# Kernel tuning notes

Hardware: AMD Instinct MI355X
Metric: run time of the kernel (lower is better)

The kernel has to match this reference:

```python
import jax, jax.numpy as jnp
import numpy as np

MARGIN = 1.0
SAFE_RADIUS = 4.0
B, C, H, W = 16, 48, 64, 64
N_CORR = 2048


def _normalize(x, eps=1e-12):
    # F.normalize(x, dim=0): L2-normalize over the channel axis
    return x / jnp.maximum(jnp.linalg.norm(x, axis=0, keepdims=True), eps)


def _grid_positions(h, w):
    i, j = jnp.meshgrid(jnp.arange(h, dtype=jnp.float32),
                        jnp.arange(w, dtype=jnp.float32), indexing='ij')
    return jnp.stack([i.reshape(-1), j.reshape(-1)], axis=0)


def _per_image(df1, df2, att1, att2, ids, fp2):
    c, h1, w1 = df1.shape
    _, h2, w2 = df2.shape
    all_d1 = _normalize(df1.reshape(c, -1))   # [c, h1*w1]
    all_d2 = _normalize(df2.reshape(c, -1))   # [c, h2*w2]

    d1 = all_d1[:, ids]                       # [c, n] gathered anchors
    s1 = att1.reshape(-1)[ids]                # [n]
    d2 = _normalize(df2[:, fp2[0], fp2[1]])   # [c, n] gathered positives

    positive_distance = 2.0 - 2.0 * jnp.sum(d1 * d2, axis=0)  # [n]

    # hard-negative mining in image 2
    grid2 = _grid_positions(h2, w2)           # [2, h2*w2]
    pd2 = jnp.max(jnp.abs(fp2.astype(jnp.float32)[:, :, None] - grid2[:, None, :]), axis=0)
    out2 = (pd2 > SAFE_RADIUS).astype(df1.dtype)            # [n, h2*w2]
    dm2 = 2.0 - 2.0 * jnp.einsum('cn,cm->nm', d1, all_d2)   # [n, h2*w2]
    neg2 = jnp.min(dm2 + (1.0 - out2) * 10.0, axis=1)       # [n]

    # hard-negative mining in image 1
    grid1 = _grid_positions(h1, w1)
    fp1 = grid1[:, ids]                                      # [2, n]
    pd1 = jnp.max(jnp.abs(fp1[:, :, None] - grid1[:, None, :]), axis=0)
    out1 = (pd1 > SAFE_RADIUS).astype(df1.dtype)
    dm1 = 2.0 - 2.0 * jnp.einsum('cn,cm->nm', d2, all_d1)
    neg1 = jnp.min(dm1 + (1.0 - out1) * 10.0, axis=1)

    diff = positive_distance - jnp.minimum(neg1, neg2)
    s2 = att2[0, fp2[0], fp2[1]]
    w = s1 * s2
    return jnp.sum(w * jax.nn.relu(MARGIN + diff)) / jnp.sum(w)


def setup_inputs() -> dict:
    key = jax.random.key(0)
    k1, k2, k3, k4, k5, k6 = jax.random.split(key, 6)
    return {
        'x1_encoded': jax.random.normal(k1, (B, C, H, W), dtype=jnp.float32),
        'x2_encoded': jax.random.normal(k2, (B, C, H, W), dtype=jnp.float32),
        'attentions1': jax.random.uniform(k3, (B, 1, H, W), dtype=jnp.float32),
        'attentions2': jax.random.uniform(k4, (B, 1, H, W), dtype=jnp.float32),
        'ids': jax.random.randint(k5, (B, N_CORR), 0, H * W),
        'fmap_pos2': jax.random.randint(k6, (B, 2, N_CORR), 0, H),
    }


def reference(x1_encoded, x2_encoded, attentions1, attentions2, ids, fmap_pos2):
    per_image = jax.vmap(_per_image)(x1_encoded, x2_encoded, attentions1,
                                     attentions2, ids, fmap_pos2)
    return jnp.mean(per_image).reshape(1)
```

## Files before the change

### kernel.cpp

```cpp
#include <hip/hip_runtime.h>
#include <stdint.h>

#define BB 16
#define HW 4096
#define NC 2048
#define KHW 72
#define KB 144

typedef __attribute__((ext_vector_type(8))) __bf16 bf16x8;
typedef __attribute__((ext_vector_type(8))) short short8;
typedef __attribute__((ext_vector_type(4))) float floatx4;

static __device__ __forceinline__ unsigned short f2bf(float f) {
    unsigned u = __builtin_bit_cast(unsigned, f);
    unsigned r = u + 0x7fffu + ((u >> 16) & 1u);
    return (unsigned short)(r >> 16);
}

#define GLD16(g, l) __builtin_amdgcn_global_load_lds((const __attribute__((address_space(1))) void*)(g), (__attribute__((address_space(3))) void*)(l), 16, 0, 0)
#define GLD4(g, l)  __builtin_amdgcn_global_load_lds((const __attribute__((address_space(1))) void*)(g), (__attribute__((address_space(3))) void*)(l), 4, 0, 0)

__global__ void prep_db(const float* __restrict__ x1, const float* __restrict__ x2,
                        unsigned short* __restrict__ dbp) {
    int gid = blockIdx.x * 256 + threadIdx.x;
    int img = gid >> 16;
    int rem = gid & 65535;
    int b = rem >> 12;
    int p = rem & (HW - 1);
    const float* x = img ? x2 : x1;
    const float* col = x + (size_t)b * 48 * HW + p;
    float v[48]; float s = 0.f;
#pragma unroll
    for (int c = 0; c < 48; ++c) { v[c] = col[c * HW]; s = fmaf(v[c], v[c], s); }
    float r = 1.f / fmaxf(sqrtf(s), 1e-12f);
    unsigned short* dst = dbp + ((size_t)(img * BB + b) * HW + p) * KHW;
#pragma unroll
    for (int ch = 0; ch < 6; ++ch) {
        union { unsigned u[4]; floatx4 f; } pk;
#pragma unroll
        for (int d = 0; d < 4; ++d) {
            int c = ch * 8 + d * 2;
            pk.u[d] = (unsigned)f2bf(v[c] * r) | ((unsigned)f2bf(v[c + 1] * r) << 16);
        }
        *(floatx4*)(dst + ch * 8) = pk.f;
    }
    floatx4 z = {0.f, 0.f, 0.f, 0.f};
#pragma unroll
    for (int ch = 6; ch < 9; ++ch) *(floatx4*)(dst + ch * 8) = z;
}

__global__ void sortq_kernel(const int* __restrict__ ids, const int* __restrict__ fp2,
                             int* __restrict__ perm, int* __restrict__ qcol_s,
                             int* __restrict__ aqpack) {
    int seg = blockIdx.x;
    int dir = seg >> 4, b = seg & 15;
    int tid = threadIdx.x;
    __shared__ int hist[64], base[64];
    if (tid < 64) hist[tid] = 0;
    __syncthreads();
#pragma unroll
    for (int k = 0; k < 8; ++k) {
        int n = k * 256 + tid;
        int idv = ids[b * NC + n];
        int i2 = fp2[b * 2 * NC + n];
        int qi = (dir == 0) ? i2 : (idv >> 6);
        atomicAdd(&hist[qi], 1);
    }
    __syncthreads();
    if (tid == 0) {
        int run = 0;
        for (int k = 0; k < 64; ++k) { base[k] = run; run += hist[k]; }
    }
    __syncthreads();
#pragma unroll
    for (int k = 0; k < 8; ++k) {
        int n = k * 256 + tid;
        int idv = ids[b * NC + n];
        int i2 = fp2[b * 2 * NC + n];
        int j2 = fp2[b * 2 * NC + NC + n];
        int qi, qj, qcol;
        if (dir == 0) { qi = i2; qj = j2; qcol = idv; }
        else          { qi = idv >> 6; qj = idv & 63; qcol = i2 * 64 + j2; }
        int slot = atomicAdd(&base[qi], 1);
        perm[seg * NC + slot] = n;
        qcol_s[seg * NC + slot] = qcol;
        aqpack[seg * NC + slot] = (qi << 8) | qj;
    }
}

static __device__ __forceinline__ void dma_tile(const unsigned char* g, unsigned char* l,
                                                int wave, int lane) {
#pragma unroll
    for (int rr = 0; rr < 4; ++rr)
        GLD16(g + rr * 4096 + wave * 1024 + lane * 16, l + rr * 4096 + wave * 1024);
#pragma unroll
    for (int rr = 0; rr < 2; ++rr)
        GLD4(g + 16384 + rr * 1024 + wave * 256 + lane * 4, l + 16384 + rr * 1024 + wave * 256);
}

__global__ __launch_bounds__(256, 4) void maxscore_mfma(
    const unsigned short* __restrict__ dbp,
    const int* __restrict__ perm, const int* __restrict__ qcol_s,
    const int* __restrict__ aqpack, unsigned int* __restrict__ maxs2enc) {
    __shared__ __align__(16) unsigned char smem[36864];

    int tid = threadIdx.x, wave = tid >> 6, lane = tid & 63;
    int quad = lane >> 4, cl = lane & 15;
    int gid = blockIdx.x;
    int seg = gid & 31, dir = seg >> 4, b = seg & 15;
    int rest = gid >> 5, mtile = rest & 7, nq = rest >> 3;
    int qbase = mtile * 256;
    int dbimg = 1 - dir;

    const unsigned char* dbQ = (const unsigned char*)(dbp + (size_t)(dir * BB + b) * HW * KHW);
    short8 afr[4][2];
#pragma unroll
    for (int t = 0; t < 4; ++t) {
        int slot = qbase + wave * 64 + t * 16 + cl;
        int qc = qcol_s[seg * NC + slot];
        const unsigned char* src = dbQ + (size_t)qc * KB;
        afr[t][0] = *(const short8*)(src + quad * 16);
        afr[t][1] = *(const short8*)(src + 64 + quad * 16);
    }
    float qif[4][4], qjc[4][4];
    float cl_f = (float)cl;
#pragma unroll
    for (int t = 0; t < 4; ++t)
#pragma unroll
        for (int r = 0; r < 4; ++r) {
            int slot = qbase + wave * 64 + t * 16 + quad * 4 + r;
            int ap = aqpack[seg * NC + slot];
            qif[t][r] = (float)(ap >> 8);
            qjc[t][r] = (float)(ap & 255) - cl_f;
        }
    int wb = seg * NC + qbase + wave * 64;
    int qimin = __builtin_amdgcn_readfirstlane(aqpack[wb] >> 8);
    int qimax = __builtin_amdgcn_readfirstlane(aqpack[wb + 63] >> 8);

    const unsigned char* dsrc =
        (const unsigned char*)(dbp + ((size_t)(dbimg * BB + b) * HW + nq * 1024) * KHW);
    dma_tile(dsrc, smem, wave, lane);

    const floatx4 zf = {0.f, 0.f, 0.f, 0.f};
    float mx[4][4];
#pragma unroll
    for (int t = 0; t < 4; ++t)
#pragma unroll
        for (int r = 0; r < 4; ++r) mx[t][r] = -1e30f;

    for (int tile = 0; tile < 8; ++tile) {
        unsigned char* buf = smem + (tile & 1) * 18432;
        __syncthreads();
        if (tile + 1 < 8)
            dma_tile(dsrc + (tile + 1) * 18432, smem + ((tile + 1) & 1) * 18432, wave, lane);
        int mi0 = (nq * 1024 + tile * 128) >> 6;
#pragma unroll
        for (int half = 0; half < 2; ++half) {
            int mi = mi0 + half;
            bool active = (mi >= qimin - 4) && (mi <= qimax + 4);
            if (active) {
                float mi_f = (float)mi;
                bool rowok[4][4];
#pragma unroll
                for (int t = 0; t < 4; ++t)
#pragma unroll
                    for (int r = 0; r < 4; ++r)
                        rowok[t][r] = fabsf(qif[t][r] - mi_f) > 4.0f;
#pragma unroll
                for (int js = 0; js < 4; ++js) {
                    int sub = half * 4 + js;
                    float jj = (float)(js * 16);
                    short8 b0 = *(const short8*)(buf + (sub * 16 + cl) * KB + quad * 16);
                    short8 b1 = *(const short8*)(buf + (sub * 16 + cl) * KB + 64 + quad * 16);
#pragma unroll
                    for (int t = 0; t < 4; ++t) {
                        floatx4 acc = __builtin_amdgcn_mfma_f32_16x16x32_bf16(
                            __builtin_bit_cast(bf16x8, afr[t][0]),
                            __builtin_bit_cast(bf16x8, b0), zf, 0, 0, 0);
                        acc = __builtin_amdgcn_mfma_f32_16x16x32_bf16(
                            __builtin_bit_cast(bf16x8, afr[t][1]),
                            __builtin_bit_cast(bf16x8, b1), acc, 0, 0, 0);
#pragma unroll
                        for (int r = 0; r < 4; ++r) {
                            float dj = qjc[t][r] - jj;
                            bool ok = rowok[t][r] || (fabsf(dj) > 4.0f);
                            mx[t][r] = ok ? fmaxf(mx[t][r], acc[r]) : mx[t][r];
                        }
                    }
                }
            } else {
#pragma unroll
                for (int js = 0; js < 4; ++js) {
                    int sub = half * 4 + js;
                    short8 b0 = *(const short8*)(buf + (sub * 16 + cl) * KB + quad * 16);
                    short8 b1 = *(const short8*)(buf + (sub * 16 + cl) * KB + 64 + quad * 16);
#pragma unroll
                    for (int t = 0; t < 4; ++t) {
                        floatx4 acc = __builtin_amdgcn_mfma_f32_16x16x32_bf16(
                            __builtin_bit_cast(bf16x8, afr[t][0]),
                            __builtin_bit_cast(bf16x8, b0), zf, 0, 0, 0);
                        acc = __builtin_amdgcn_mfma_f32_16x16x32_bf16(
                            __builtin_bit_cast(bf16x8, afr[t][1]),
                            __builtin_bit_cast(bf16x8, b1), acc, 0, 0, 0);
#pragma unroll
                        for (int r = 0; r < 4; ++r)
                            mx[t][r] = fmaxf(mx[t][r], acc[r]);
                    }
                }
            }
        }
    }

#pragma unroll
    for (int t = 0; t < 4; ++t)
#pragma unroll
        for (int r = 0; r < 4; ++r) {
            float v = mx[t][r];
            v = fmaxf(v, __shfl_xor(v, 1, 16));
            v = fmaxf(v, __shfl_xor(v, 2, 16));
            v = fmaxf(v, __shfl_xor(v, 4, 16));
            v = fmaxf(v, __shfl_xor(v, 8, 16));
            mx[t][r] = v;
        }
    if (cl == 0) {
#pragma unroll
        for (int t = 0; t < 4; ++t)
#pragma unroll
            for (int r = 0; r < 4; ++r) {
                int slot = qbase + wave * 64 + t * 16 + quad * 4 + r;
                int orig = perm[seg * NC + slot];
                float v = mx[t][r] + 2.0f;
                atomicMax(&maxs2enc[(size_t)seg * NC + orig],
                          __builtin_bit_cast(unsigned, v));
            }
    }
}

__global__ void loss_kernel(const float* __restrict__ att1, const float* __restrict__ att2,
                            const int* __restrict__ ids, const int* __restrict__ fp2,
                            const unsigned short* __restrict__ dbp,
                            const unsigned int* __restrict__ maxs2enc,
                            float* __restrict__ pnum, float* __restrict__ pden) {
    int b = blockIdx.x >> 3, chunk = blockIdx.x & 7;
    int tid = threadIdx.x;
    int n = chunk * 256 + tid;
    int idv = ids[b * NC + n];
    int i2 = fp2[b * 2 * NC + n], j2 = fp2[b * 2 * NC + NC + n];
    const uint4* a4 = (const uint4*)(dbp + ((size_t)(0 * BB + b) * HW + idv) * KHW);
    const uint4* b4 = (const uint4*)(dbp + ((size_t)(1 * BB + b) * HW + i2 * 64 + j2) * KHW);
    float dot = 0.f;
#pragma unroll
    for (int i = 0; i < 6; ++i) {
        uint4 xa = a4[i], xb = b4[i];
        const unsigned* xu = (const unsigned*)&xa;
        const unsigned* yu = (const unsigned*)&xb;
#pragma unroll
        for (int w = 0; w < 4; ++w) {
            float xl = __builtin_bit_cast(float, xu[w] << 16);
            float xh = __builtin_bit_cast(float, xu[w] & 0xffff0000u);
            float yl = __builtin_bit_cast(float, yu[w] << 16);
            float yh = __builtin_bit_cast(float, yu[w] & 0xffff0000u);
            dot = fmaf(xl, yl, fmaf(xh, yh, dot));
        }
    }
    float m0 = __builtin_bit_cast(float, maxs2enc[(size_t)(0 * BB + b) * NC + n]) - 2.0f;
    float m1 = __builtin_bit_cast(float, maxs2enc[(size_t)(1 * BB + b) * NC + n]) - 2.0f;
    float ms = fmaxf(m0, m1);
    float diff = (2.f - 2.f * dot) - (2.f - 2.f * ms);
    float w = att1[b * HW + idv] * att2[b * HW + i2 * 64 + j2];
    float num = w * fmaxf(0.f, 1.f + diff);
    float den = w;
    __shared__ float sn[256], sd[256];
    sn[tid] = num; sd[tid] = den;
    __syncthreads();
    for (int s = 128; s > 0; s >>= 1) {
        if (tid < s) { sn[tid] += sn[tid + s]; sd[tid] += sd[tid + s]; }
        __syncthreads();
    }
    if (tid == 0) { pnum[blockIdx.x] = sn[0]; pden[blockIdx.x] = sd[0]; }
}

__global__ void final_kernel(const float* __restrict__ pnum, const float* __restrict__ pden,
                             float* __restrict__ out) {
    int tid = threadIdx.x;
    __shared__ float r[16];
    if (tid < 16) {
        float n = 0.f, d = 0.f;
#pragma unroll
        for (int c = 0; c < 8; ++c) { n += pnum[tid * 8 + c]; d += pden[tid * 8 + c]; }
        r[tid] = n / d;
    }
    __syncthreads();
    if (tid == 0) {
        float s = 0.f;
#pragma unroll
        for (int k = 0; k < 16; ++k) s += r[k];
        out[0] = s * (1.f / BB);
    }
}

extern "C" void kernel_launch(void* const* d_in, const int* in_sizes, int n_in,
                              void* d_out, int out_size, void* d_ws, size_t ws_size,
                              hipStream_t stream) {
    const float* x1  = (const float*)d_in[0];
    const float* x2  = (const float*)d_in[1];
    const float* att1 = (const float*)d_in[2];
    const float* att2 = (const float*)d_in[3];
    const int* ids   = (const int*)d_in[4];
    const int* fp2   = (const int*)d_in[5];
    float* out = (float*)d_out;

    unsigned char* w = (unsigned char*)d_ws;
    unsigned short* dbp = (unsigned short*)(w + 0);
    int* perm    = (int*)(w + 18874368);
    int* qcol_s  = (int*)(w + 19136512);
    int* aqpack  = (int*)(w + 19398656);
    unsigned int* maxs2enc = (unsigned int*)(w + 19660800);
    float* pnum  = (float*)(w + 19922944);
    float* pden  = (float*)(w + 19923456);

    prep_db<<<dim3(512), dim3(256), 0, stream>>>(x1, x2, dbp);
    sortq_kernel<<<dim3(32), dim3(256), 0, stream>>>(ids, fp2, perm, qcol_s, aqpack);
    hipMemsetAsync(maxs2enc, 0, 32 * NC * sizeof(unsigned int), stream);
    maxscore_mfma<<<dim3(1024), dim3(256), 0, stream>>>(dbp, perm, qcol_s, aqpack, maxs2enc);
    loss_kernel<<<dim3(128), dim3(256), 0, stream>>>(att1, att2, ids, fp2, dbp, maxs2enc, pnum, pden);
    final_kernel<<<dim3(1), dim3(64), 0, stream>>>(pnum, pden, out);
}
```

Before: 139.0 us.

## Fuse prep, sort and memset launches; halve score tile for more blocks

Three pre-pass launches (normalize/convert, query sort, and the memset of the max buffer) are merged into a single kernel whose block ranges dispatch to each role, removing launch gaps. The max-score kernel now covers 512 database columns per block instead of 1024, using 64-column tiles and half the LDS. The grid doubles to 2048 blocks and launch bounds rise to 8 blocks per CU for occupancy. The trade-off is twice as many query fragment loads across blocks and smaller DMA tiles per sync.

New measurement: 431.1 us. 210% more time.

```diff
diff --git a/kernel.cpp b/kernel.cpp
--- a/kernel.cpp
+++ b/kernel.cpp
@@ -20,89 +20,95 @@
 #define GLD16(g, l) __builtin_amdgcn_global_load_lds((const __attribute__((address_space(1))) void*)(g), (__attribute__((address_space(3))) void*)(l), 16, 0, 0)
 #define GLD4(g, l)  __builtin_amdgcn_global_load_lds((const __attribute__((address_space(1))) void*)(g), (__attribute__((address_space(3))) void*)(l), 4, 0, 0)
 
-__global__ void prep_db(const float* __restrict__ x1, const float* __restrict__ x2,
-                        unsigned short* __restrict__ dbp) {
-    int gid = blockIdx.x * 256 + threadIdx.x;
-    int img = gid >> 16;
-    int rem = gid & 65535;
-    int b = rem >> 12;
-    int p = rem & (HW - 1);
-    const float* x = img ? x2 : x1;
-    const float* col = x + (size_t)b * 48 * HW + p;
-    float v[48]; float s = 0.f;
-#pragma unroll
-    for (int c = 0; c < 48; ++c) { v[c] = col[c * HW]; s = fmaf(v[c], v[c], s); }
-    float r = 1.f / fmaxf(sqrtf(s), 1e-12f);
-    unsigned short* dst = dbp + ((size_t)(img * BB + b) * HW + p) * KHW;
-#pragma unroll
-    for (int ch = 0; ch < 6; ++ch) {
-        union { unsigned u[4]; floatx4 f; } pk;
-#pragma unroll
-        for (int d = 0; d < 4; ++d) {
-            int c = ch * 8 + d * 2;
-            pk.u[d] = (unsigned)f2bf(v[c] * r) | ((unsigned)f2bf(v[c + 1] * r) << 16);
-        }
-        *(floatx4*)(dst + ch * 8) = pk.f;
-    }
-    floatx4 z = {0.f, 0.f, 0.f, 0.f};
-#pragma unroll
-    for (int ch = 6; ch < 9; ++ch) *(floatx4*)(dst + ch * 8) = z;
-}
-
-__global__ void sortq_kernel(const int* __restrict__ ids, const int* __restrict__ fp2,
-                             int* __restrict__ perm, int* __restrict__ qcol_s,
-                             int* __restrict__ aqpack) {
-    int seg = blockIdx.x;
-    int dir = seg >> 4, b = seg & 15;
-    int tid = threadIdx.x;
+__global__ void prep_fused(const float* __restrict__ x1, const float* __restrict__ x2,
+                           const int* __restrict__ ids, const int* __restrict__ fp2,
+                           unsigned short* __restrict__ dbp,
+                           int* __restrict__ perm, int* __restrict__ qcol_s,
+                           int* __restrict__ aqpack, unsigned int* __restrict__ maxs2enc) {
+    int bid = blockIdx.x, tid = threadIdx.x;
     __shared__ int hist[64], base[64];
-    if (tid < 64) hist[tid] = 0;
-    __syncthreads();
-#pragma unroll
-    for (int k = 0; k < 8; ++k) {
-        int n = k * 256 + tid;
-        int idv = ids[b * NC + n];
-        int i2 = fp2[b * 2 * NC + n];
-        int qi = (dir == 0) ? i2 : (idv >> 6);
-        atomicAdd(&hist[qi], 1);
-    }
-    __syncthreads();
-    if (tid == 0) {
-        int run = 0;
-        for (int k = 0; k < 64; ++k) { base[k] = run; run += hist[k]; }
-    }
-    __syncthreads();
-#pragma unroll
-    for (int k = 0; k < 8; ++k) {
-        int n = k * 256 + tid;
-        int idv = ids[b * NC + n];
-        int i2 = fp2[b * 2 * NC + n];
-        int j2 = fp2[b * 2 * NC + NC + n];
-        int qi, qj, qcol;
-        if (dir == 0) { qi = i2; qj = j2; qcol = idv; }
-        else          { qi = idv >> 6; qj = idv & 63; qcol = i2 * 64 + j2; }
-        int slot = atomicAdd(&base[qi], 1);
-        perm[seg * NC + slot] = n;
-        qcol_s[seg * NC + slot] = qcol;
-        aqpack[seg * NC + slot] = (qi << 8) | qj;
-    }
-}
-
-static __device__ __forceinline__ void dma_tile(const unsigned char* g, unsigned char* l,
-                                                int wave, int lane) {
-#pragma unroll
-    for (int rr = 0; rr < 4; ++rr)
-        GLD16(g + rr * 4096 + wave * 1024 + lane * 16, l + rr * 4096 + wave * 1024);
+    if (bid < 512) {
+        int gid = bid * 256 + tid;
+        int img = gid >> 16;
+        int rem = gid & 65535;
+        int b = rem >> 12;
+        int p = rem & (HW - 1);
+        const float* x = img ? x2 : x1;
+        const float* col = x + (size_t)b * 48 * HW + p;
+        float v[48]; float s = 0.f;
+#pragma unroll
+        for (int c = 0; c < 48; ++c) { v[c] = col[c * HW]; s = fmaf(v[c], v[c], s); }
+        float r = 1.f / fmaxf(sqrtf(s), 1e-12f);
+        unsigned short* dst = dbp + ((size_t)(img * BB + b) * HW + p) * KHW;
+#pragma unroll
+        for (int ch = 0; ch < 6; ++ch) {
+            union { unsigned u[4]; floatx4 f; } pk;
+#pragma unroll
+            for (int d = 0; d < 4; ++d) {
+                int c = ch * 8 + d * 2;
+                pk.u[d] = (unsigned)f2bf(v[c] * r) | ((unsigned)f2bf(v[c + 1] * r) << 16);
+            }
+            *(floatx4*)(dst + ch * 8) = pk.f;
+        }
+        floatx4 z = {0.f, 0.f, 0.f, 0.f};
+#pragma unroll
+        for (int ch = 6; ch < 9; ++ch) *(floatx4*)(dst + ch * 8) = z;
+    } else if (bid < 544) {
+        int seg = bid - 512;
+        int dir = seg >> 4, b = seg & 15;
+        if (tid < 64) hist[tid] = 0;
+        __syncthreads();
+#pragma unroll
+        for (int k = 0; k < 8; ++k) {
+            int n = k * 256 + tid;
+            int idv = ids[b * NC + n];
+            int i2 = fp2[b * 2 * NC + n];
+            int qi = (dir == 0) ? i2 : (idv >> 6);
+            atomicAdd(&hist[qi], 1);
+        }
+        __syncthreads();
+        if (tid == 0) {
+            int run = 0;
+            for (int k = 0; k < 64; ++k) { base[k] = run; run += hist[k]; }
+        }
+        __syncthreads();
+#pragma unroll
+        for (int k = 0; k < 8; ++k) {
+            int n = k * 256 + tid;
+            int idv = ids[b * NC + n];
+            int i2 = fp2[b * 2 * NC + n];
+            int j2 = fp2[b * 2 * NC + NC + n];
+            int qi, qj, qcol;
+            if (dir == 0) { qi = i2; qj = j2; qcol = idv; }
+            else          { qi = idv >> 6; qj = idv & 63; qcol = i2 * 64 + j2; }
+            int slot = atomicAdd(&base[qi], 1);
+            perm[seg * NC + slot] = n;
+            qcol_s[seg * NC + slot] = qcol;
+            aqpack[seg * NC + slot] = (qi << 8) | qj;
+        }
+    } else {
+        int t = (bid - 544) * 256 + tid;
+        uint4* p = (uint4*)maxs2enc;
+        uint4 z = {0u, 0u, 0u, 0u};
+#pragma unroll
+        for (int k = 0; k < 8; ++k) p[k * 2048 + t] = z;
+    }
+}
+
+static __device__ __forceinline__ void dma64(const unsigned char* g, unsigned char* l,
+                                             int wave, int lane) {
+    int wo = wave * 2304;
 #pragma unroll
     for (int rr = 0; rr < 2; ++rr)
-        GLD4(g + 16384 + rr * 1024 + wave * 256 + lane * 4, l + 16384 + rr * 1024 + wave * 256);
-}
-
-__global__ __launch_bounds__(256, 4) void maxscore_mfma(
+        GLD16(g + wo + rr * 1024 + lane * 16, l + wo + rr * 1024);
+    GLD4(g + wo + 2048 + lane * 4, l + wo + 2048);
+}
+
+__global__ __launch_bounds__(256, 8) void maxscore_mfma(
     const unsigned short* __restrict__ dbp,
     const int* __restrict__ perm, const int* __restrict__ qcol_s,
     const int* __restrict__ aqpack, unsigned int* __restrict__ maxs2enc) {
-    __shared__ __align__(16) unsigned char smem[36864];
+    __shared__ __align__(16) unsigned char smem[18432];
 
     int tid = threadIdx.x, wave = tid >> 6, lane = tid & 63;
     int quad = lane >> 4, cl = lane & 15;
@@ -138,8 +144,8 @@
     int qimax = __builtin_amdgcn_readfirstlane(aqpack[wb + 63] >> 8);
 
     const unsigned char* dsrc =
-        (const unsigned char*)(dbp + ((size_t)(dbimg * BB + b) * HW + nq * 1024) * KHW);
-    dma_tile(dsrc, smem, wave, lane);
+        (const unsigned char*)(dbp + ((size_t)(dbimg * BB + b) * HW + nq * 512) * KHW);
+    dma64(dsrc, smem, wave, lane);
 
     const floatx4 zf = {0.f, 0.f, 0.f, 0.f};
     float mx[4][4];
@@ -149,63 +155,57 @@
         for (int r = 0; r < 4; ++r) mx[t][r] = -1e30f;
 
     for (int tile = 0; tile < 8; ++tile) {
-        unsigned char* buf = smem + (tile & 1) * 18432;
+        unsigned char* buf = smem + (tile & 1) * 9216;
         __syncthreads();
         if (tile + 1 < 8)
-            dma_tile(dsrc + (tile + 1) * 18432, smem + ((tile + 1) & 1) * 18432, wave, lane);
-        int mi0 = (nq * 1024 + tile * 128) >> 6;
-#pragma unroll
-        for (int half = 0; half < 2; ++half) {
-            int mi = mi0 + half;
-            bool active = (mi >= qimin - 4) && (mi <= qimax + 4);
-            if (active) {
-                float mi_f = (float)mi;
-                bool rowok[4][4];
-#pragma unroll
-                for (int t = 0; t < 4; ++t)
-#pragma unroll
-                    for (int r = 0; r < 4; ++r)
-                        rowok[t][r] = fabsf(qif[t][r] - mi_f) > 4.0f;
-#pragma unroll
-                for (int js = 0; js < 4; ++js) {
-                    int sub = half * 4 + js;
-                    float jj = (float)(js * 16);
-                    short8 b0 = *(const short8*)(buf + (sub * 16 + cl) * KB + quad * 16);
-                    short8 b1 = *(const short8*)(buf + (sub * 16 + cl) * KB + 64 + quad * 16);
-#pragma unroll
-                    for (int t = 0; t < 4; ++t) {
-                        floatx4 acc = __builtin_amdgcn_mfma_f32_16x16x32_bf16(
-                            __builtin_bit_cast(bf16x8, afr[t][0]),
-                            __builtin_bit_cast(bf16x8, b0), zf, 0, 0, 0);
-                        acc = __builtin_amdgcn_mfma_f32_16x16x32_bf16(
-                            __builtin_bit_cast(bf16x8, afr[t][1]),
-                            __builtin_bit_cast(bf16x8, b1), acc, 0, 0, 0);
-#pragma unroll
-                        for (int r = 0; r < 4; ++r) {
-                            float dj = qjc[t][r] - jj;
-                            bool ok = rowok[t][r] || (fabsf(dj) > 4.0f);
-                            mx[t][r] = ok ? fmaxf(mx[t][r], acc[r]) : mx[t][r];
-                        }
+            dma64(dsrc + (tile + 1) * 9216, smem + ((tile + 1) & 1) * 9216, wave, lane);
+        int mi = nq * 8 + tile;
+        bool active = (mi >= qimin - 4) && (mi <= qimax + 4);
+        if (active) {
+            float mi_f = (float)mi;
+            bool rowok[4][4];
+#pragma unroll
+            for (int t = 0; t < 4; ++t)
+#pragma unroll
+                for (int r = 0; r < 4; ++r)
+                    rowok[t][r] = fabsf(qif[t][r] - mi_f) > 4.0f;
+#pragma unroll
+            for (int js = 0; js < 4; ++js) {
+                float jj = (float)(js * 16);
+                short8 b0 = *(const short8*)(buf + (js * 16 + cl) * KB + quad * 16);
+                short8 b1 = *(const short8*)(buf + (js * 16 + cl) * KB + 64 + quad * 16);
+#pragma unroll
+                for (int t = 0; t < 4; ++t) {
+                    floatx4 acc = __builtin_amdgcn_mfma_f32_16x16x32_bf16(
+                        __builtin_bit_cast(bf16x8, afr[t][0]),
+                        __builtin_bit_cast(bf16x8, b0), zf, 0, 0, 0);
+                    acc = __builtin_amdgcn_mfma_f32_16x16x32_bf16(
+                        __builtin_bit_cast(bf16x8, afr[t][1]),
+                        __builtin_bit_cast(bf16x8, b1), acc, 0, 0, 0);
+#pragma unroll
+                    for (int r = 0; r < 4; ++r) {
+                        float dj = qjc[t][r] - jj;
+                        bool ok = rowok[t][r] || (fabsf(dj) > 4.0f);
+                        mx[t][r] = ok ? fmaxf(mx[t][r], acc[r]) : mx[t][r];
                     }
                 }
-            } else {
-#pragma unroll
-                for (int js = 0; js < 4; ++js) {
-                    int sub = half * 4 + js;
-                    short8 b0 = *(const short8*)(buf + (sub * 16 + cl) * KB + quad * 16);
-                    short8 b1 = *(const short8*)(buf + (sub * 16 + cl) * KB + 64 + quad * 16);
-#pragma unroll
-                    for (int t = 0; t < 4; ++t) {
-                        floatx4 acc = __builtin_amdgcn_mfma_f32_16x16x32_bf16(
-                            __builtin_bit_cast(bf16x8, afr[t][0]),
-                            __builtin_bit_cast(bf16x8, b0), zf, 0, 0, 0);
-                        acc = __builtin_amdgcn_mfma_f32_16x16x32_bf16(
-                            __builtin_bit_cast(bf16x8, afr[t][1]),
-                            __builtin_bit_cast(bf16x8, b1), acc, 0, 0, 0);
-#pragma unroll
-                        for (int r = 0; r < 4; ++r)
-                            mx[t][r] = fmaxf(mx[t][r], acc[r]);
-                    }
+            }
+        } else {
+#pragma unroll
+            for (int js = 0; js < 4; ++js) {
+                short8 b0 = *(const short8*)(buf + (js * 16 + cl) * KB + quad * 16);
+                short8 b1 = *(const short8*)(buf + (js * 16 + cl) * KB + 64 + quad * 16);
+#pragma unroll
+                for (int t = 0; t < 4; ++t) {
+                    floatx4 acc = __builtin_amdgcn_mfma_f32_16x16x32_bf16(
+                        __builtin_bit_cast(bf16x8, afr[t][0]),
+                        __builtin_bit_cast(bf16x8, b0), zf, 0, 0, 0);
+                    acc = __builtin_amdgcn_mfma_f32_16x16x32_bf16(
+                        __builtin_bit_cast(bf16x8, afr[t][1]),
+                        __builtin_bit_cast(bf16x8, b1), acc, 0, 0, 0);
+#pragma unroll
+                    for (int r = 0; r < 4; ++r)
+                        mx[t][r] = fmaxf(mx[t][r], acc[r]);
                 }
             }
         }
@@ -319,10 +319,9 @@
     float* pnum  = (float*)(w + 19922944);
     float* pden  = (float*)(w + 19923456);
 
-    prep_db<<<dim3(512), dim3(256), 0, stream>>>(x1, x2, dbp);
-    sortq_kernel<<<dim3(32), dim3(256), 0, stream>>>(ids, fp2, perm, qcol_s, aqpack);
-    hipMemsetAsync(maxs2enc, 0, 32 * NC * sizeof(unsigned int), stream);
-    maxscore_mfma<<<dim3(1024), dim3(256), 0, stream>>>(dbp, perm, qcol_s, aqpack, maxs2enc);
+    prep_fused<<<dim3(552), dim3(256), 0, stream>>>(x1, x2, ids, fp2, dbp,
+                                                    perm, qcol_s, aqpack, maxs2enc);
+    maxscore_mfma<<<dim3(2048), dim3(256), 0, stream>>>(dbp, perm, qcol_s, aqpack, maxs2enc);
     loss_kernel<<<dim3(128), dim3(256), 0, stream>>>(att1, att2, ids, fp2, dbp, maxs2enc, pnum, pden);
     final_kernel<<<dim3(1), dim3(64), 0, stream>>>(pnum, pden, out);
 }
```
